# Kernel optimization log

Hardware: AMD Instinct MI355X
Metric: run time of the kernel (lower is better)

The kernel has to match this reference:

```python
import jax, jax.numpy as jnp
import numpy as np

N = 500_000        # nodes
F = 128            # node feature dim
E = 4_000_000      # edges
B = 4              # graphs in batch
COORD_RANGE = 256.0
VOXEL = 8.0        # voxel_size (same per dim, from init size=[8,8,8])
G = int(COORD_RANGE // VOXEL)   # 32 voxels per dim
V = B * G * G * G               # fixed number of voxel slots
EFFECTIVE_RADIUS = 8.0          # Cartesian max_value


def setup_inputs() -> dict:
    key = jax.random.key(0)
    k1, k2, k3 = jax.random.split(key, 3)
    x = jax.random.normal(k1, (N, F), dtype=jnp.float32)
    pos = jax.random.uniform(k2, (N, 3), dtype=jnp.float32) * COORD_RANGE
    # sorted segment ids: B contiguous graphs
    batch = ((jnp.arange(N) * B) // N).astype(jnp.int32)
    edge_index = jax.random.randint(k3, (2, E), 0, N, dtype=jnp.int64)
    return {"x": x, "pos": pos, "batch": batch, "edge_index": edge_index}


def reference(x, pos, batch, edge_index):
    # ---- voxel_grid: assign each node to a (batch, voxel) cluster ----
    v = jnp.clip(jnp.floor(pos / VOXEL).astype(jnp.int32), 0, G - 1)  # [N,3]
    vid = batch * (G * G * G) + v[:, 0] * (G * G) + v[:, 1] * G + v[:, 2]  # [N]

    # ---- max_pool: scatter-max features, mean positions per cluster ----
    pooled_x = jax.ops.segment_max(x, vid, num_segments=V)            # [V,F]
    count = jax.ops.segment_sum(jnp.ones((N,), x.dtype), vid, num_segments=V)  # [V]
    occupied = count > 0
    pooled_x = jnp.where(occupied[:, None], pooled_x, 0.0)
    pooled_pos = jax.ops.segment_sum(pos, vid, num_segments=V) / jnp.maximum(count, 1.0)[:, None]  # [V,3]

    # ---- remap edges to clusters; mask self-loops (coalesce approximated by mask) ----
    src = vid[edge_index[0]]  # [E]
    dst = vid[edge_index[1]]  # [E]
    edge_mask = src != dst
    new_edge_index = jnp.stack([src, dst])  # [2,E]

    # ---- Cartesian(cat=False, norm=True, max_value=effective_radius) ----
    cart = pooled_pos[dst] - pooled_pos[src]                 # [E,3]
    edge_attr = cart / (2.0 * EFFECTIVE_RADIUS) + 0.5
    edge_attr = jnp.where(edge_mask[:, None], edge_attr, 0.0)

    return pooled_x, pooled_pos, new_edge_index, edge_attr, edge_mask
```

## Files before the change

kernel.cpp:

```cpp
#include <hip/hip_runtime.h>

#define NN 500000
#define FF 128
#define EE 4000000
#define BB 4
#define GG 32
#define VV (BB * GG * GG * GG)

#define OUT_X    0
#define OUT_POS  (VV * FF)
#define OUT_EIDX (OUT_POS + VV * 3)
#define OUT_ATTR (OUT_EIDX + 2 * EE)
#define OUT_MASK (OUT_ATTR + 3 * EE)

__global__ __launch_bounds__(256) void vid_kernel(
    const float* __restrict__ pos, const int* __restrict__ batch,
    int* __restrict__ vid, unsigned int* __restrict__ cnt,
    float* __restrict__ pos_sum)
{
    int n = blockIdx.x * 256 + threadIdx.x;
    if (n >= NN) return;
    float px = pos[3 * n + 0], py = pos[3 * n + 1], pz = pos[3 * n + 2];
    int vx = min(max((int)floorf(px * 0.125f), 0), GG - 1);
    int vy = min(max((int)floorf(py * 0.125f), 0), GG - 1);
    int vz = min(max((int)floorf(pz * 0.125f), 0), GG - 1);
    int v = batch[n] * (GG * GG * GG) + vx * (GG * GG) + vy * GG + vz;
    vid[n] = v;
    atomicAdd(&cnt[v], 1u);
    atomicAdd(&pos_sum[3 * v + 0], px);
    atomicAdd(&pos_sum[3 * v + 1], py);
    atomicAdd(&pos_sum[3 * v + 2], pz);
}

__global__ __launch_bounds__(256) void scan_local_kernel(
    const unsigned int* __restrict__ cnt, unsigned int* __restrict__ offs,
    unsigned int* __restrict__ bsum)
{
    __shared__ unsigned int s[256];
    int i = blockIdx.x * 256 + threadIdx.x;
    unsigned int val = cnt[i];
    s[threadIdx.x] = val;
    __syncthreads();
    for (int d = 1; d < 256; d <<= 1) {
        unsigned int t = (threadIdx.x >= d) ? s[threadIdx.x - d] : 0u;
        __syncthreads();
        s[threadIdx.x] += t;
        __syncthreads();
    }
    offs[i] = s[threadIdx.x] - val;
    if (threadIdx.x == 255) bsum[blockIdx.x] = s[255];
}

__global__ __launch_bounds__(512) void scan_bsum_kernel(unsigned int* __restrict__ bsum)
{
    __shared__ unsigned int s[512];
    unsigned int val = bsum[threadIdx.x];
    s[threadIdx.x] = val;
    __syncthreads();
    for (int d = 1; d < 512; d <<= 1) {
        unsigned int t = (threadIdx.x >= d) ? s[threadIdx.x - d] : 0u;
        __syncthreads();
        s[threadIdx.x] += t;
        __syncthreads();
    }
    bsum[threadIdx.x] = s[threadIdx.x] - val;
}

__global__ __launch_bounds__(256) void scan_add_kernel(
    unsigned int* __restrict__ offs, const unsigned int* __restrict__ bsum,
    unsigned int* __restrict__ cursor)
{
    int i = blockIdx.x * 256 + threadIdx.x;
    unsigned int o = offs[i] + bsum[blockIdx.x];
    offs[i] = o;
    cursor[i] = o;
}

__global__ __launch_bounds__(256) void scatter_kernel(
    const int* __restrict__ vid, unsigned int* __restrict__ cursor,
    unsigned int* __restrict__ order)
{
    int n = blockIdx.x * 256 + threadIdx.x;
    if (n >= NN) return;
    unsigned int p = atomicAdd(&cursor[vid[n]], 1u);
    order[p] = n;
}

__global__ __launch_bounds__(256) void pool_kernel(
    const float* __restrict__ x, const unsigned int* __restrict__ order,
    const unsigned int* __restrict__ offs, const unsigned int* __restrict__ cnt,
    float* __restrict__ out_x)
{
    int w = threadIdx.x >> 6;
    int lane = threadIdx.x & 63;
    int v = blockIdx.x * 4 + w;
    unsigned int start = offs[v];
    unsigned int c = cnt[v];
    float2 m = make_float2(0.0f, 0.0f);
    if (c) {
        m.x = -INFINITY; m.y = -INFINITY;
        for (unsigned int k = 0; k < c; ++k) {
            unsigned int node = order[start + k];
            float2 val = ((const float2*)(x + (size_t)node * FF))[lane];
            m.x = fmaxf(m.x, val.x);
            m.y = fmaxf(m.y, val.y);
        }
    }
    ((float2*)(out_x + (size_t)v * FF))[lane] = m;
}

__global__ __launch_bounds__(256) void fix_pos_kernel(
    float* __restrict__ out_pos, const float* __restrict__ pos_sum,
    const unsigned int* __restrict__ cnt)
{
    int v = blockIdx.x * 256 + threadIdx.x;
    float inv = 1.0f / fmaxf((float)cnt[v], 1.0f);
    out_pos[3 * v + 0] = pos_sum[3 * v + 0] * inv;
    out_pos[3 * v + 1] = pos_sum[3 * v + 1] * inv;
    out_pos[3 * v + 2] = pos_sum[3 * v + 2] * inv;
}

__global__ __launch_bounds__(256) void edge_kernel(
    const int* __restrict__ eidx, const int* __restrict__ vid,
    const float* __restrict__ pooled_pos, float* __restrict__ out)
{
    int e = blockIdx.x * 256 + threadIdx.x;
    if (e >= EE) return;
    int sv = vid[eidx[e]];
    int dv = vid[eidx[EE + e]];
    bool m = (sv != dv);
    out[OUT_EIDX + e] = (float)sv;
    out[OUT_EIDX + EE + e] = (float)dv;
    float ax = 0.0f, ay = 0.0f, az = 0.0f;
    if (m) {
        ax = (pooled_pos[3 * dv + 0] - pooled_pos[3 * sv + 0]) * 0.0625f + 0.5f;
        ay = (pooled_pos[3 * dv + 1] - pooled_pos[3 * sv + 1]) * 0.0625f + 0.5f;
        az = (pooled_pos[3 * dv + 2] - pooled_pos[3 * sv + 2]) * 0.0625f + 0.5f;
    }
    out[OUT_ATTR + 3 * e + 0] = ax;
    out[OUT_ATTR + 3 * e + 1] = ay;
    out[OUT_ATTR + 3 * e + 2] = az;
    out[OUT_MASK + e] = m ? 1.0f : 0.0f;
}

extern "C" void kernel_launch(void* const* d_in, const int* in_sizes, int n_in,
                              void* d_out, int out_size, void* d_ws, size_t ws_size,
                              hipStream_t stream)
{
    const float* x     = (const float*)d_in[0];
    const float* pos   = (const float*)d_in[1];
    const int*   batch = (const int*)d_in[2];
    const int*   eidx  = (const int*)d_in[3];
    float* out = (float*)d_out;

    char* ws = (char*)d_ws;
    unsigned int* cnt     = (unsigned int*)(ws + 0);
    float*        pos_sum = (float*)(ws + 524288);
    int*          vid     = (int*)(ws + 2097152);
    unsigned int* offs    = (unsigned int*)(ws + 4097152);
    unsigned int* cursor  = (unsigned int*)(ws + 4621440);
    unsigned int* bsum    = (unsigned int*)(ws + 5145728);
    unsigned int* order   = (unsigned int*)(ws + 5147776);

    hipMemsetAsync(d_ws, 0, 2097152, stream);

    vid_kernel<<<(NN + 255) / 256, 256, 0, stream>>>(pos, batch, vid, cnt, pos_sum);
    scan_local_kernel<<<VV / 256, 256, 0, stream>>>(cnt, offs, bsum);
    scan_bsum_kernel<<<1, 512, 0, stream>>>(bsum);
    scan_add_kernel<<<VV / 256, 256, 0, stream>>>(offs, bsum, cursor);
    scatter_kernel<<<(NN + 255) / 256, 256, 0, stream>>>(vid, cursor, order);
    pool_kernel<<<VV / 4, 256, 0, stream>>>(x, order, offs, cnt, out + OUT_X);
    fix_pos_kernel<<<VV / 256, 256, 0, stream>>>(out + OUT_POS, pos_sum, cnt);
    edge_kernel<<<(EE + 255) / 256, 256, 0, stream>>>(eidx, vid, out + OUT_POS, out);
}
```

Baseline: 669.4 us.

## Fuse position mean into pool kernel, widen pooling loads, stage edge attrs in LDS

The per-node float atomics for position sums are removed. Pooled positions are now computed inside the pool kernel through a wave reduction over the sorted node list, and the separate fix_pos kernel and part of the memset are dropped. The pool kernel now has four lane groups each handle a different node with float4 loads, to get more memory parallelism per wave. The edge kernel stages its 3-float attributes in shared memory so the global writes are coalesced. This adds shuffle reductions and a barrier in the edge kernel, and the change in summation order can alter float rounding of the pooled positions.

Measured after the change: 554.4 us. 17.2% less time.

```diff
diff --git a/kernel.cpp b/kernel.cpp
--- a/kernel.cpp
+++ b/kernel.cpp
@@ -15,8 +15,7 @@
 
 __global__ __launch_bounds__(256) void vid_kernel(
     const float* __restrict__ pos, const int* __restrict__ batch,
-    int* __restrict__ vid, unsigned int* __restrict__ cnt,
-    float* __restrict__ pos_sum)
+    int* __restrict__ vid, unsigned int* __restrict__ cnt)
 {
     int n = blockIdx.x * 256 + threadIdx.x;
     if (n >= NN) return;
@@ -27,9 +26,6 @@
     int v = batch[n] * (GG * GG * GG) + vx * (GG * GG) + vy * GG + vz;
     vid[n] = v;
     atomicAdd(&cnt[v], 1u);
-    atomicAdd(&pos_sum[3 * v + 0], px);
-    atomicAdd(&pos_sum[3 * v + 1], py);
-    atomicAdd(&pos_sum[3 * v + 2], pz);
 }
 
 __global__ __launch_bounds__(256) void scan_local_kernel(
@@ -87,45 +83,72 @@
 }
 
 __global__ __launch_bounds__(256) void pool_kernel(
-    const float* __restrict__ x, const unsigned int* __restrict__ order,
+    const float* __restrict__ x, const float* __restrict__ pos,
+    const unsigned int* __restrict__ order,
     const unsigned int* __restrict__ offs, const unsigned int* __restrict__ cnt,
-    float* __restrict__ out_x)
+    float* __restrict__ out_x, float* __restrict__ out_pos)
 {
     int w = threadIdx.x >> 6;
     int lane = threadIdx.x & 63;
+    int g = lane >> 4;
+    int fl = lane & 15;
     int v = blockIdx.x * 4 + w;
     unsigned int start = offs[v];
     unsigned int c = cnt[v];
-    float2 m = make_float2(0.0f, 0.0f);
-    if (c) {
-        m.x = -INFINITY; m.y = -INFINITY;
-        for (unsigned int k = 0; k < c; ++k) {
-            unsigned int node = order[start + k];
-            float2 val = ((const float2*)(x + (size_t)node * FF))[lane];
-            m.x = fmaxf(m.x, val.x);
-            m.y = fmaxf(m.y, val.y);
+
+    float4 mlo = make_float4(-INFINITY, -INFINITY, -INFINITY, -INFINITY);
+    float4 mhi = mlo;
+    float sx = 0.0f, sy = 0.0f, sz = 0.0f;
+
+    for (unsigned int base = 0; base < c; base += 64) {
+        unsigned int rem = min(c - base, 64u);
+        unsigned int idx = (lane < rem) ? order[start + base + lane] : 0u;
+        if (lane < rem) {
+            const float* pp = pos + 3 * (size_t)idx;
+            sx += pp[0]; sy += pp[1]; sz += pp[2];
         }
-    }
-    ((float2*)(out_x + (size_t)v * FF))[lane] = m;
-}
-
-__global__ __launch_bounds__(256) void fix_pos_kernel(
-    float* __restrict__ out_pos, const float* __restrict__ pos_sum,
-    const unsigned int* __restrict__ cnt)
-{
-    int v = blockIdx.x * 256 + threadIdx.x;
-    float inv = 1.0f / fmaxf((float)cnt[v], 1.0f);
-    out_pos[3 * v + 0] = pos_sum[3 * v + 0] * inv;
-    out_pos[3 * v + 1] = pos_sum[3 * v + 1] * inv;
-    out_pos[3 * v + 2] = pos_sum[3 * v + 2] * inv;
+        for (unsigned int k = (unsigned int)g; k < rem; k += 4) {
+            unsigned int n = __shfl(idx, (int)k);
+            const float4* row = (const float4*)(x + (size_t)n * FF);
+            float4 a = row[fl];
+            float4 b = row[fl + 16];
+            mlo.x = fmaxf(mlo.x, a.x); mlo.y = fmaxf(mlo.y, a.y);
+            mlo.z = fmaxf(mlo.z, a.z); mlo.w = fmaxf(mlo.w, a.w);
+            mhi.x = fmaxf(mhi.x, b.x); mhi.y = fmaxf(mhi.y, b.y);
+            mhi.z = fmaxf(mhi.z, b.z); mhi.w = fmaxf(mhi.w, b.w);
+        }
+    }
+
+    #define MERGE(f) f = fmaxf(f, __shfl_xor(f, 16)); f = fmaxf(f, __shfl_xor(f, 32));
+    MERGE(mlo.x) MERGE(mlo.y) MERGE(mlo.z) MERGE(mlo.w)
+    MERGE(mhi.x) MERGE(mhi.y) MERGE(mhi.z) MERGE(mhi.w)
+    #undef MERGE
+
+    float4 res = (lane < 16) ? mlo : mhi;
+    if (c == 0) res = make_float4(0.0f, 0.0f, 0.0f, 0.0f);
+    if (lane < 32)
+        ((float4*)(out_x + (size_t)v * FF))[lane] = res;
+
+    for (int d = 1; d < 64; d <<= 1) {
+        sx += __shfl_xor(sx, d);
+        sy += __shfl_xor(sy, d);
+        sz += __shfl_xor(sz, d);
+    }
+    if (lane == 0) {
+        float inv = 1.0f / fmaxf((float)c, 1.0f);
+        out_pos[3 * v + 0] = sx * inv;
+        out_pos[3 * v + 1] = sy * inv;
+        out_pos[3 * v + 2] = sz * inv;
+    }
 }
 
 __global__ __launch_bounds__(256) void edge_kernel(
     const int* __restrict__ eidx, const int* __restrict__ vid,
     const float* __restrict__ pooled_pos, float* __restrict__ out)
 {
-    int e = blockIdx.x * 256 + threadIdx.x;
-    if (e >= EE) return;
+    __shared__ float sattr[768];
+    int e0 = blockIdx.x * 256;
+    int e = e0 + threadIdx.x;
     int sv = vid[eidx[e]];
     int dv = vid[eidx[EE + e]];
     bool m = (sv != dv);
@@ -137,10 +160,15 @@
         ay = (pooled_pos[3 * dv + 1] - pooled_pos[3 * sv + 1]) * 0.0625f + 0.5f;
         az = (pooled_pos[3 * dv + 2] - pooled_pos[3 * sv + 2]) * 0.0625f + 0.5f;
     }
-    out[OUT_ATTR + 3 * e + 0] = ax;
-    out[OUT_ATTR + 3 * e + 1] = ay;
-    out[OUT_ATTR + 3 * e + 2] = az;
+    sattr[3 * threadIdx.x + 0] = ax;
+    sattr[3 * threadIdx.x + 1] = ay;
+    sattr[3 * threadIdx.x + 2] = az;
     out[OUT_MASK + e] = m ? 1.0f : 0.0f;
+    __syncthreads();
+    float* dst = out + OUT_ATTR + (size_t)3 * e0;
+    #pragma unroll
+    for (int i = 0; i < 3; ++i)
+        dst[i * 256 + threadIdx.x] = sattr[i * 256 + threadIdx.x];
 }
 
 extern "C" void kernel_launch(void* const* d_in, const int* in_sizes, int n_in,
@@ -155,21 +183,20 @@
 
     char* ws = (char*)d_ws;
     unsigned int* cnt     = (unsigned int*)(ws + 0);
-    float*        pos_sum = (float*)(ws + 524288);
-    int*          vid     = (int*)(ws + 2097152);
-    unsigned int* offs    = (unsigned int*)(ws + 4097152);
-    unsigned int* cursor  = (unsigned int*)(ws + 4621440);
-    unsigned int* bsum    = (unsigned int*)(ws + 5145728);
-    unsigned int* order   = (unsigned int*)(ws + 5147776);
-
-    hipMemsetAsync(d_ws, 0, 2097152, stream);
-
-    vid_kernel<<<(NN + 255) / 256, 256, 0, stream>>>(pos, batch, vid, cnt, pos_sum);
+    int*          vid     = (int*)(ws + 524288);
+    unsigned int* offs    = (unsigned int*)(ws + 2524288);
+    unsigned int* cursor  = (unsigned int*)(ws + 3048576);
+    unsigned int* bsum    = (unsigned int*)(ws + 3572864);
+    unsigned int* order   = (unsigned int*)(ws + 3574912);
+
+    hipMemsetAsync(d_ws, 0, 524288, stream);
+
+    vid_kernel<<<(NN + 255) / 256, 256, 0, stream>>>(pos, batch, vid, cnt);
     scan_local_kernel<<<VV / 256, 256, 0, stream>>>(cnt, offs, bsum);
     scan_bsum_kernel<<<1, 512, 0, stream>>>(bsum);
     scan_add_kernel<<<VV / 256, 256, 0, stream>>>(offs, bsum, cursor);
     scatter_kernel<<<(NN + 255) / 256, 256, 0, stream>>>(vid, cursor, order);
-    pool_kernel<<<VV / 4, 256, 0, stream>>>(x, order, offs, cnt, out + OUT_X);
-    fix_pos_kernel<<<VV / 256, 256, 0, stream>>>(out + OUT_POS, pos_sum, cnt);
+    pool_kernel<<<VV / 4, 256, 0, stream>>>(x, pos, order, offs, cnt,
+                                            out + OUT_X, out + OUT_POS);
     edge_kernel<<<(EE + 255) / 256, 256, 0, stream>>>(eidx, vid, out + OUT_POS, out);
 }
```
